# Kernel tuning notes

Measured on AMD Instinct MI355X. Metric: run time of the kernel, lower is better.

The kernel has to match this reference:

```python
import jax, jax.numpy as jnp
import numpy as np

CROP_H = 7
CROP_W = 7
EXTRAP = 0.0  # module hardcodes 0 when calling CropAndResizeFunction


def _crop_and_resize(image, boxes, box_ind):
    """TF-style crop_and_resize.
    image: (N,C,H,W) float; boxes: (M,4) normalized (y1,x1,y2,x2); box_ind: (M,) int32.
    Returns (M,C,CROP_H,CROP_W).
    """
    N, C, H, W = image.shape
    dt = image.dtype
    y1, x1, y2, x2 = boxes[:, 0], boxes[:, 1], boxes[:, 2], boxes[:, 3]
    ii = jnp.arange(CROP_H, dtype=dt)
    jj = jnp.arange(CROP_W, dtype=dt)
    # sample coordinates in feature-map space, shape (M, CROP_H) / (M, CROP_W)
    y = y1[:, None] * (H - 1) + ii[None, :] * ((y2 - y1) * (H - 1) / (CROP_H - 1))[:, None]
    x = x1[:, None] * (W - 1) + jj[None, :] * ((x2 - x1) * (W - 1) / (CROP_W - 1))[:, None]
    valid_y = (y >= 0) & (y <= H - 1)
    valid_x = (x >= 0) & (x <= W - 1)
    yt_f = jnp.floor(y)
    xt_f = jnp.floor(x)
    y_lerp = y - yt_f  # (M, oh)
    x_lerp = x - xt_f  # (M, ow)
    yt = jnp.clip(yt_f, 0, H - 1).astype(jnp.int32)
    yb = jnp.clip(jnp.ceil(y), 0, H - 1).astype(jnp.int32)
    xl = jnp.clip(xt_f, 0, W - 1).astype(jnp.int32)
    xr = jnp.clip(jnp.ceil(x), 0, W - 1).astype(jnp.int32)
    img = jnp.transpose(image, (0, 2, 3, 1))  # (N,H,W,C) for clean gather
    b = box_ind[:, None, None]                # (M,1,1)
    tl = img[b, yt[:, :, None], xl[:, None, :]]  # (M,oh,ow,C)
    tr = img[b, yt[:, :, None], xr[:, None, :]]
    bl = img[b, yb[:, :, None], xl[:, None, :]]
    br = img[b, yb[:, :, None], xr[:, None, :]]
    xl_w = x_lerp[:, None, :, None]
    top = tl + (tr - tl) * xl_w
    bot = bl + (br - bl) * xl_w
    out = top + (bot - top) * y_lerp[:, :, None, None]
    valid = (valid_y[:, :, None] & valid_x[:, None, :])[..., None]
    out = jnp.where(valid, out, jnp.asarray(EXTRAP, dt))
    return jnp.transpose(out, (0, 3, 1, 2))  # (M,C,oh,ow)


def setup_inputs() -> dict:
    key = jax.random.key(0)
    k0, k1, k2, k3, k4, k5 = jax.random.split(key, 6)
    N, C, H, W = 2, 256, 200, 304
    M = 2048
    scale = 0.0625  # 1/16
    Himg, Wimg = H / scale, W / scale
    featuremap = jax.random.normal(k0, (N, C, H, W), dtype=jnp.float32)
    x1 = jax.random.uniform(k1, (M, 1), minval=0.0, maxval=Wimg - 260.0)
    y1 = jax.random.uniform(k2, (M, 1), minval=0.0, maxval=Himg - 260.0)
    bw = jax.random.uniform(k3, (M, 1), minval=32.0, maxval=256.0)
    bh = jax.random.uniform(k4, (M, 1), minval=32.0, maxval=256.0)
    ids = jax.random.randint(k5, (M, 1), 0, N).astype(jnp.float32)
    rois = jnp.concatenate([ids, x1, y1, x1 + bw, y1 + bh], axis=1)
    return {"featuremap": featuremap, "rois": rois, "spatial_scale": jnp.float32(scale)}


def reference(featuremap, rois, spatial_scale):
    H, W = featuremap.shape[2], featuremap.shape[3]
    boxes = rois[:, 1:5] * spatial_scale
    box_ind = rois[:, 0].astype(jnp.int32)
    x1, y1, x2, y2 = boxes[:, 0], boxes[:, 1], boxes[:, 2], boxes[:, 3]
    spacing_w = (x2 - x1) / CROP_W
    spacing_h = (y2 - y1) / CROP_H
    nx0 = (x1 + spacing_w / 2 - 0.5) / (W - 1)
    ny0 = (y1 + spacing_h / 2 - 0.5) / (H - 1)
    nw = spacing_w * (CROP_W - 1) / (W - 1)
    nh = spacing_h * (CROP_H - 1) / (H - 1)
    boxes_n = jnp.stack([ny0, nx0, ny0 + nh, nx0 + nw], axis=1)
    return _crop_and_resize(featuremap, boxes_n, box_ind)
```

## Files before the change

### kernel.cpp

```cpp
#include <hip/hip_runtime.h>

#define RA_C   256
#define RA_H   200
#define RA_W   304
#define RA_HW  (RA_H * RA_W)
#define RA_CHW (RA_C * RA_HW)
#define CROPN  7
#define CROP2  (CROPN * CROPN)
#define PER_M  (RA_C * CROP2)

__global__ __launch_bounds__(256) void roialign_kernel(
    const float* __restrict__ fm, const float* __restrict__ rois,
    const float* __restrict__ scale_p, float* __restrict__ out)
{
    __shared__ int   s_offT[CROPN], s_offB[CROPN];
    __shared__ float s_ylerp[CROPN], s_vy[CROPN];
    __shared__ int   s_xl[CROPN], s_xr[CROPN];
    __shared__ float s_xlerp[CROPN], s_vx[CROPN];
    __shared__ int   s_imgbase;

    const int t = threadIdx.x;
    const int m = blockIdx.x;

    if (t < 2 * CROPN) {
        #pragma clang fp contract(off)
        {
            const float scale = scale_p[0];
            const float* r = rois + (size_t)m * 5;
            const int axis = (t < CROPN) ? 0 : 1;
            const int k = axis ? (t - CROPN) : t;
            float lo, hi, szm1;
            if (axis == 0) { lo = r[2] * scale; hi = r[4] * scale; szm1 = (float)(RA_H - 1); }
            else           { lo = r[1] * scale; hi = r[3] * scale; szm1 = (float)(RA_W - 1); }
            float sp   = (hi - lo) / 7.0f;
            float n0   = (lo + sp * 0.5f - 0.5f) / szm1;
            float nsz  = sp * 6.0f / szm1;
            float b2   = n0 + nsz;
            float d    = (b2 - n0) * szm1 / 6.0f;
            float coord = n0 * szm1 + (float)k * d;
            float fl = floorf(coord);
            float ce = ceilf(coord);
            float lerp = coord - fl;
            int lo_i = (int)fminf(fmaxf(fl, 0.0f), szm1);
            int hi_i = (int)fminf(fmaxf(ce, 0.0f), szm1);
            float valid = (coord >= 0.0f && coord <= szm1) ? 1.0f : 0.0f;
            if (axis == 0) {
                s_offT[k] = lo_i * RA_W; s_offB[k] = hi_i * RA_W;
                s_ylerp[k] = lerp; s_vy[k] = valid;
            } else {
                s_xl[k] = lo_i; s_xr[k] = hi_i;
                s_xlerp[k] = lerp; s_vx[k] = valid;
            }
        }
    }
    if (t == 63) {
        s_imgbase = (int)rois[(size_t)m * 5] * RA_CHW;
    }
    __syncthreads();

    const float* __restrict__ img = fm + s_imgbase;
    float* __restrict__ outm = out + (size_t)m * PER_M;

    for (int e = t; e < PER_M; e += 256) {
        int c  = e / CROP2;
        int ij = e - c * CROP2;
        int i  = ij / CROPN;
        int j  = ij - i * CROPN;
        const float* __restrict__ p = img + (size_t)c * RA_HW;
        const int ot = s_offT[i], ob = s_offB[i];
        const int xl = s_xl[j],  xr = s_xr[j];
        const float xw = s_xlerp[j];
        const float yw = s_ylerp[i];
        const float v  = s_vy[i] * s_vx[j];
        float tl = p[ot + xl];
        float tr = p[ot + xr];
        float bl = p[ob + xl];
        float br = p[ob + xr];
        float top = tl + (tr - tl) * xw;
        float bot = bl + (br - bl) * xw;
        float res = (top + (bot - top) * yw) * v;
        outm[e] = res;
    }
}

extern "C" void kernel_launch(void* const* d_in, const int* in_sizes, int n_in,
                              void* d_out, int out_size, void* d_ws, size_t ws_size,
                              hipStream_t stream) {
    const float* fm    = (const float*)d_in[0];
    const float* rois  = (const float*)d_in[1];
    const float* scale = (const float*)d_in[2];
    float* out = (float*)d_out;
    const int M = in_sizes[1] / 5;
    roialign_kernel<<<dim3(M), dim3(256), 0, stream>>>(fm, rois, scale, out);
}
```

Before: 296.7 us.

## Tile work by ROI group and channel slice with XCD-aware block mapping

Each block now handles 32 ROIs across an 8-channel slice instead of one ROI across all 256 channels. The block index is decoded so that each of the 8 XCDs handles a fixed set of channel slices, which keeps the feature-map channels an XCD touches in its own L2 and improves cache reuse of the gathered pixels. The cost is 32x more per-block setup (coordinate computation for 32 ROIs), more scattered output writes, and a requirement that M be a multiple of 32.

```diff
diff --git a/kernel.cpp b/kernel.cpp
--- a/kernel.cpp
+++ b/kernel.cpp
@@ -7,31 +7,45 @@
 #define RA_CHW (RA_C * RA_HW)
 #define CROPN  7
 #define CROP2  (CROPN * CROPN)
-#define PER_M  (RA_C * CROP2)
+#define OUT_M  (RA_C * CROP2)
+#define BC     8
+#define BM     32
+#define PER_BLK (BM * BC * CROP2)
 
 __global__ __launch_bounds__(256) void roialign_kernel(
     const float* __restrict__ fm, const float* __restrict__ rois,
     const float* __restrict__ scale_p, float* __restrict__ out)
 {
-    __shared__ int   s_offT[CROPN], s_offB[CROPN];
-    __shared__ float s_ylerp[CROPN], s_vy[CROPN];
-    __shared__ int   s_xl[CROPN], s_xr[CROPN];
-    __shared__ float s_xlerp[CROPN], s_vx[CROPN];
-    __shared__ int   s_imgbase;
+    __shared__ int   s_offT[BM][CROPN], s_offB[BM][CROPN];
+    __shared__ float s_ylerp[BM][CROPN], s_vy[BM][CROPN];
+    __shared__ int   s_xl[BM][CROPN], s_xr[BM][CROPN];
+    __shared__ float s_xlerp[BM][CROPN], s_vx[BM][CROPN];
+    __shared__ int   s_imgbase[BM];
 
     const int t = threadIdx.x;
-    const int m = blockIdx.x;
 
-    if (t < 2 * CROPN) {
+    const int bid   = blockIdx.x;
+    const int numBG = gridDim.x >> 5;
+    const int xcd   = bid & 7;
+    const int r     = bid >> 3;
+    const int cgl   = r / numBG;
+    const int bg    = r - cgl * numBG;
+    const int c0    = (xcd * 4 + cgl) * BC;
+    const int m0    = bg * BM;
+
+    for (int task = t; task < BM * 2 * CROPN; task += 256) {
         #pragma clang fp contract(off)
         {
+            const int mm  = task / (2 * CROPN);
+            const int k14 = task - mm * (2 * CROPN);
+            const int axis = (k14 >= CROPN) ? 1 : 0;
+            const int k = axis ? (k14 - CROPN) : k14;
             const float scale = scale_p[0];
-            const float* r = rois + (size_t)m * 5;
-            const int axis = (t < CROPN) ? 0 : 1;
-            const int k = axis ? (t - CROPN) : t;
+            const float* rr = rois + (size_t)(m0 + mm) * 5;
+            if (k14 == 0) s_imgbase[mm] = (int)rr[0] * RA_CHW;
             float lo, hi, szm1;
-            if (axis == 0) { lo = r[2] * scale; hi = r[4] * scale; szm1 = (float)(RA_H - 1); }
-            else           { lo = r[1] * scale; hi = r[3] * scale; szm1 = (float)(RA_W - 1); }
+            if (axis == 0) { lo = rr[2] * scale; hi = rr[4] * scale; szm1 = (float)(RA_H - 1); }
+            else           { lo = rr[1] * scale; hi = rr[3] * scale; szm1 = (float)(RA_W - 1); }
             float sp   = (hi - lo) / 7.0f;
             float n0   = (lo + sp * 0.5f - 0.5f) / szm1;
             float nsz  = sp * 6.0f / szm1;
@@ -45,33 +59,30 @@
             int hi_i = (int)fminf(fmaxf(ce, 0.0f), szm1);
             float valid = (coord >= 0.0f && coord <= szm1) ? 1.0f : 0.0f;
             if (axis == 0) {
-                s_offT[k] = lo_i * RA_W; s_offB[k] = hi_i * RA_W;
-                s_ylerp[k] = lerp; s_vy[k] = valid;
+                s_offT[mm][k] = lo_i * RA_W; s_offB[mm][k] = hi_i * RA_W;
+                s_ylerp[mm][k] = lerp; s_vy[mm][k] = valid;
             } else {
-                s_xl[k] = lo_i; s_xr[k] = hi_i;
-                s_xlerp[k] = lerp; s_vx[k] = valid;
+                s_xl[mm][k] = lo_i; s_xr[mm][k] = hi_i;
+                s_xlerp[mm][k] = lerp; s_vx[mm][k] = valid;
             }
         }
     }
-    if (t == 63) {
-        s_imgbase = (int)rois[(size_t)m * 5] * RA_CHW;
-    }
     __syncthreads();
 
-    const float* __restrict__ img = fm + s_imgbase;
-    float* __restrict__ outm = out + (size_t)m * PER_M;
-
-    for (int e = t; e < PER_M; e += 256) {
-        int c  = e / CROP2;
-        int ij = e - c * CROP2;
-        int i  = ij / CROPN;
-        int j  = ij - i * CROPN;
-        const float* __restrict__ p = img + (size_t)c * RA_HW;
-        const int ot = s_offT[i], ob = s_offB[i];
-        const int xl = s_xl[j],  xr = s_xr[j];
-        const float xw = s_xlerp[j];
-        const float yw = s_ylerp[i];
-        const float v  = s_vy[i] * s_vx[j];
+    for (int e = t; e < PER_BLK; e += 256) {
+        int mm  = e / (BC * CROP2);
+        int rem = e - mm * (BC * CROP2);
+        int cc  = rem / CROP2;
+        int ij  = rem - cc * CROP2;
+        int i   = ij / CROPN;
+        int j   = ij - i * CROPN;
+        const float* __restrict__ p =
+            fm + (size_t)s_imgbase[mm] + (size_t)(c0 + cc) * RA_HW;
+        const int ot = s_offT[mm][i], ob = s_offB[mm][i];
+        const int xl = s_xl[mm][j],  xr = s_xr[mm][j];
+        const float xw = s_xlerp[mm][j];
+        const float yw = s_ylerp[mm][i];
+        const float v  = s_vy[mm][i] * s_vx[mm][j];
         float tl = p[ot + xl];
         float tr = p[ot + xr];
         float bl = p[ob + xl];
@@ -79,7 +90,7 @@
         float top = tl + (tr - tl) * xw;
         float bot = bl + (br - bl) * xw;
         float res = (top + (bot - top) * yw) * v;
-        outm[e] = res;
+        out[(size_t)(m0 + mm) * OUT_M + (size_t)(c0 + cc) * CROP2 + ij] = res;
     }
 }
 
@@ -91,5 +102,6 @@
     const float* scale = (const float*)d_in[2];
     float* out = (float*)d_out;
     const int M = in_sizes[1] / 5;
-    roialign_kernel<<<dim3(M), dim3(256), 0, stream>>>(fm, rois, scale, out);
+    const int numBG = M / BM;
+    roialign_kernel<<<dim3(32 * numBG), dim3(256), 0, stream>>>(fm, rois, scale, out);
 }
```

New measurement: 294.4 us. No clear change (-0.8%).
